# Optimization experiments

Measured on AMD Instinct MI355X. Metric: run time of the kernel, lower is better.

Reference implementation:

```python
import jax, jax.numpy as jnp
import numpy as np
from jax import lax

D_MODEL = 1024
D_STATE = 128
HEADDIM = 64
EXPAND = 2
NGROUPS = 1
CHUNK = 256
D_INNER = EXPAND * D_MODEL          # 2048
D_SSM = D_INNER                      # d_ssm defaults to d_inner
NHEADS = D_SSM // HEADDIM            # 32
CONV_DIM = D_SSM + 2 * NGROUPS * D_STATE   # 2304
D_IN_PROJ = 2 * D_INNER + 2 * NGROUPS * D_STATE + NHEADS  # 4384 -> d_mlp = 0
BATCH = 2
SEQLEN = 2048
EPS = 1e-5


def setup_inputs() -> dict:
    key = jax.random.key(0)
    ks = jax.random.split(key, 9)
    u = jax.random.normal(ks[0], (BATCH, SEQLEN, D_MODEL), jnp.float32)
    # indices into left-padded (len = SEQLEN+1) sequence; 0 selects the zero pad
    conv_indices = jax.random.randint(ks[1], (BATCH, 4 * SEQLEN), 0, SEQLEN + 1)
    W_in = jax.random.normal(ks[2], (D_IN_PROJ, D_MODEL), jnp.float32) / np.sqrt(D_MODEL).astype(np.float32)
    conv_w = jax.random.normal(ks[3], (CONV_DIM, 4), jnp.float32) * 0.2
    conv_b = jax.random.normal(ks[4], (CONV_DIM,), jnp.float32) * 0.02
    # dt_bias init exactly as the module: inverse-softplus of dt in [dt_min, dt_max]
    dt = jnp.exp(jax.random.uniform(ks[5], (NHEADS,), jnp.float32) * (np.log(0.1) - np.log(0.001)) + np.log(0.001))
    dt = jnp.clip(dt, 1e-4)
    dt_bias = dt + jnp.log(-jnp.expm1(-dt))
    A_log = jnp.log(jax.random.uniform(ks[6], (NHEADS,), jnp.float32, minval=1.0, maxval=16.0))
    D = jnp.ones((NHEADS,), jnp.float32)
    norm_w = jnp.ones((D_SSM,), jnp.float32)
    W_out = jax.random.normal(ks[7], (D_MODEL, D_INNER), jnp.float32) / np.sqrt(D_INNER).astype(np.float32)
    return dict(u=u, conv_indices=conv_indices, W_in=W_in, conv_w=conv_w, conv_b=conv_b,
                dt_bias=dt_bias, A_log=A_log, D=D, norm_w=norm_w, W_out=W_out)


def _segsum(x):
    # x: (b, c, h, cs) -> (b, c, h, cs, cs); out[..., t, s] = sum_{k=s+1..t} x[..., k]
    cs = x.shape[-1]
    cx = jnp.cumsum(x, axis=-1)
    diff = cx[..., :, None] - cx[..., None, :]
    mask = jnp.tril(jnp.ones((cs, cs), dtype=bool))
    return jnp.where(mask, diff, -jnp.inf)


def _ssd(x, dt, A, Bh, Ch, D):
    # Mamba2 SSD chunked scan. x:(b,l,h,p), dt:(b,l,h), A:(h,), Bh/Ch:(b,l,h,n), D:(h,)
    b, l, h, p = x.shape
    n = Bh.shape[-1]
    c = l // CHUNK
    xr = x.reshape(b, c, CHUNK, h, p)
    dtr = dt.reshape(b, c, CHUNK, h)
    Br = Bh.reshape(b, c, CHUNK, h, n)
    Cr = Ch.reshape(b, c, CHUNK, h, n)
    dA = dtr * A                                 # (b,c,cs,h)
    Acum = jnp.cumsum(dA, axis=2)                # (b,c,cs,h)
    Lm = jnp.exp(_segsum(jnp.transpose(dA, (0, 1, 3, 2))))  # (b,c,h,cs,cs)
    dtx = xr * dtr[..., None]                    # dt-weighted inputs
    # intra-chunk (diagonal blocks)
    Yd = jnp.einsum('bcthn,bcshn,bchts,bcshp->bcthp', Cr, Br, Lm, dtx)
    # per-chunk final states
    decay_states = jnp.exp(Acum[:, :, -1:, :] - Acum)        # (b,c,cs,h)
    states = jnp.einsum('bcshn,bcsh,bcshp->bchpn', Br, decay_states, dtx)
    chunk_decay = jnp.exp(Acum[:, :, -1, :])     # (b,c,h)
    def step(h_prev, inp):
        dec, st = inp
        return h_prev * dec[..., None, None] + st, h_prev
    init = jnp.zeros((b, h, p, n), x.dtype)
    _, prev = lax.scan(step, init, (jnp.moveaxis(chunk_decay, 1, 0), jnp.moveaxis(states, 1, 0)))
    prev = jnp.moveaxis(prev, 0, 1)              # (b,c,h,p,n): state entering each chunk
    # inter-chunk (off-diagonal) contribution
    Yoff = jnp.einsum('bcthn,bchpn,bcth->bcthp', Cr, prev, jnp.exp(Acum))
    Y = Yd + Yoff + D[None, None, None, :, None] * xr
    return Y.reshape(b, l, h, p)


def reference(u, conv_indices, W_in, conv_w, conv_b, dt_bias, A_log, D, norm_w, W_out):
    b, l, _ = u.shape
    zxbcdt = u @ W_in.T                          # (b,l,4384); d_mlp == 0
    z, xBC, dt_raw = jnp.split(zxbcdt, [D_SSM, D_SSM + CONV_DIM], axis=-1)
    # tree conv: left-pad seq by 1, gather 4 tree positions per output step, depthwise conv k=4 stride=4
    xc = jnp.transpose(xBC, (0, 2, 1))           # (b, conv_dim, l)
    xp = jnp.pad(xc, ((0, 0), (0, 0), (1, 0)))
    idx = jnp.broadcast_to(conv_indices[:, None, :], (b, CONV_DIM, 4 * l))
    g = jnp.take_along_axis(xp, idx, axis=2).reshape(b, CONV_DIM, l, 4)
    conv = jnp.einsum('bclk,ck->bcl', g, conv_w) + conv_b[None, :, None]
    xBC = jax.nn.silu(jnp.transpose(conv, (0, 2, 1)))  # (b,l,conv_dim)
    x, Bm, Cm = jnp.split(xBC, [D_SSM, D_SSM + NGROUPS * D_STATE], axis=-1)
    x = x.reshape(b, l, NHEADS, HEADDIM)
    hpg = NHEADS // NGROUPS
    Bh = jnp.repeat(Bm.reshape(b, l, NGROUPS, D_STATE), hpg, axis=2)
    Ch = jnp.repeat(Cm.reshape(b, l, NGROUPS, D_STATE), hpg, axis=2)
    dt = jax.nn.softplus(dt_raw + dt_bias)       # dt_softplus=True, default dt_limit
    A = -jnp.exp(A_log.astype(jnp.float32))
    y = _ssd(x, dt, A, Bh, Ch, D).reshape(b, l, D_SSM)
    # RMSNormGated, norm_before_gate=False, group_size = d_ssm (ngroups=1)
    yz = y * jax.nn.silu(z)
    var = jnp.mean(jnp.square(yz), axis=-1, keepdims=True)
    y = yz * lax.rsqrt(var + EPS) * norm_w
    return y @ W_out.T
```

## Files before the change

kernel.cpp:

```cpp
#include <hip/hip_runtime.h>

#define BB 2
#define LL 2048
#define DMODEL 1024
#define DSSM 2048
#define NH 32
#define HD 64
#define DST 128
#define CONVD 2304
#define DPROJ 4384
#define CS 64
#define NC 32
#define BLTOT (BB*LL)

typedef short v8s __attribute__((ext_vector_type(8)));
typedef float v4f __attribute__((ext_vector_type(4)));

__device__ __forceinline__ float b2f(unsigned short h) {
  union { unsigned int u; float f; } v; v.u = ((unsigned int)h) << 16; return v.f;
}
__device__ __forceinline__ unsigned short f2b(float f) {
  union { float f; unsigned int u; } v; v.f = f;
  unsigned int u = v.u;
  return (unsigned short)((u + 0x7fffu + ((u >> 16) & 1u)) >> 16);
}
__device__ __forceinline__ v4f mfma16(v8s a, v8s b, v4f c) {
  return __builtin_amdgcn_mfma_f32_16x16x32_bf16(a, b, c, 0, 0, 0);
}
__device__ __forceinline__ void gl_lds16(const unsigned short* g, unsigned short* l) {
  __builtin_amdgcn_global_load_lds(
      (const __attribute__((address_space(1))) void*)(g),
      (__attribute__((address_space(3))) void*)(l), 16, 0, 0);
}

__global__ __launch_bounds__(256) void cvt3_kernel(
    const float* __restrict__ a, unsigned short* __restrict__ oa, int na4,
    const float* __restrict__ b, unsigned short* __restrict__ ob, int nb4,
    const float* __restrict__ c, unsigned short* __restrict__ oc, int nc4)
{
  int i = blockIdx.x * 256 + threadIdx.x;
  const float* src; unsigned short* dst; int j;
  if (i < na4) { src = a; dst = oa; j = i; }
  else if (i < na4 + nb4) { src = b; dst = ob; j = i - na4; }
  else if (i < na4 + nb4 + nc4) { src = c; dst = oc; j = i - na4 - nb4; }
  else return;
  float4 v = ((const float4*)src)[j];
  ushort4 o;
  o.x = f2b(v.x); o.y = f2b(v.y); o.z = f2b(v.z); o.w = f2b(v.w);
  ((ushort4*)dst)[j] = o;
}

template<int TN, int OUT_BF16>
__global__ __launch_bounds__(256) void gemm_bt(
    const unsigned short* __restrict__ A, const unsigned short* __restrict__ Bt,
    void* __restrict__ Cout, int M, int N, int K, int ldc)
{
  constexpr int NT = TN / 32;
  const int bm = blockIdx.x, bn = blockIdx.y;
  const int tid = threadIdx.x;
  const int wave = tid >> 6, lane = tid & 63;
  const int wm = wave & 1, wn = wave >> 1;
  const int q = lane >> 4, lr = lane & 15;

  __shared__ __align__(16) unsigned short As[128 * 64];
  __shared__ __align__(16) unsigned short Bs[TN * 64];

  v4f acc[4][NT];
#pragma unroll
  for (int i = 0; i < 4; i++)
#pragma unroll
    for (int j = 0; j < NT; j++) acc[i][j] = v4f{0.f, 0.f, 0.f, 0.f};

  const int lrow = lane >> 3;
  const int gchunk = (lane & 7) ^ lrow;

  for (int k0 = 0; k0 < K; k0 += 64) {
    __syncthreads();
#pragma unroll
    for (int it = 0; it < 4; ++it) {
      int r = wave * 32 + it * 8 + lrow;
      gl_lds16(A + (size_t)(bm * 128 + r) * K + k0 + gchunk * 8,
               &As[(wave * 32 + it * 8) * 64]);
    }
#pragma unroll
    for (int it = 0; it < TN / 32; ++it) {
      int rloc = wave * (TN / 4) + it * 8;
      int rb = bn * TN + rloc + lrow; if (rb >= N) rb = N - 1;
      gl_lds16(Bt + (size_t)rb * K + k0 + gchunk * 8, &Bs[rloc * 64]);
    }
    __syncthreads();
#pragma unroll
    for (int ks = 0; ks < 64; ks += 32) {
      const int c0 = (ks >> 3) + q;
      v8s af[4], bf[NT];
#pragma unroll
      for (int mt = 0; mt < 4; ++mt) {
        int r = wm * 64 + mt * 16 + lr;
        af[mt] = *(const v8s*)&As[r * 64 + ((c0 ^ (r & 7)) << 3)];
      }
#pragma unroll
      for (int nt = 0; nt < NT; ++nt) {
        int r = wn * (TN / 2) + nt * 16 + lr;
        bf[nt] = *(const v8s*)&Bs[r * 64 + ((c0 ^ (r & 7)) << 3)];
      }
#pragma unroll
      for (int mt = 0; mt < 4; ++mt)
#pragma unroll
        for (int nt = 0; nt < NT; ++nt)
          acc[mt][nt] = mfma16(af[mt], bf[nt], acc[mt][nt]);
    }
  }
#pragma unroll
  for (int mt = 0; mt < 4; ++mt) {
#pragma unroll
    for (int nt = 0; nt < NT; ++nt) {
      int row = bm * 128 + wm * 64 + mt * 16 + q * 4;
      int col = bn * TN + wn * (TN / 2) + nt * 16 + lr;
      if (col < N) {
#pragma unroll
        for (int r = 0; r < 4; ++r) {
          float v = acc[mt][nt][r];
          if (OUT_BF16) ((unsigned short*)Cout)[(size_t)(row + r) * ldc + col] = f2b(v);
          else          ((float*)Cout)[(size_t)(row + r) * ldc + col] = v;
        }
      }
    }
  }
}

__global__ __launch_bounds__(256) void conv_kernel(
    const unsigned short* __restrict__ C1, const int* __restrict__ cidx,
    const float* __restrict__ convw, const float* __restrict__ convb,
    const float* __restrict__ dtbias,
    unsigned short* __restrict__ x16, unsigned short* __restrict__ Bg16,
    unsigned short* __restrict__ Cg16, float* __restrict__ dtb)
{
  int bl0 = blockIdx.x * 4;
  int b = bl0 >> 11;
  int tid = threadIdx.x;
  __shared__ int idxs[16];
  if (tid < 16) {
    int tk = tid >> 2, k = tid & 3;
    idxs[tid] = cidx[b * (4 * LL) + (((bl0 + tk) & 2047) * 4) + k];
  }
  __syncthreads();
  const float4* cw4 = (const float4*)convw;
#pragma unroll
  for (int it = 0; it < 3; ++it) {
    int unit = tid + it * 256;
    if (unit >= CONVD / 4) break;
    int c4 = unit * 4;
    float4 w0 = cw4[c4], w1 = cw4[c4 + 1], w2 = cw4[c4 + 2], w3 = cw4[c4 + 3];
    float4 cb = *(const float4*)(convb + c4);
#pragma unroll
    for (int tk = 0; tk < 4; ++tk) {
      int bl = bl0 + tk;
      ushort4 rv[4];
#pragma unroll
      for (int k = 0; k < 4; ++k) {
        int iv = idxs[tk * 4 + k];
        rv[k] = (iv > 0) ? *(const ushort4*)(C1 + (size_t)(b * LL + iv - 1) * DPROJ + DSSM + c4)
                         : make_ushort4(0, 0, 0, 0);
      }
      float a0 = cb.x + b2f(rv[0].x) * w0.x + b2f(rv[1].x) * w0.y + b2f(rv[2].x) * w0.z + b2f(rv[3].x) * w0.w;
      float a1 = cb.y + b2f(rv[0].y) * w1.x + b2f(rv[1].y) * w1.y + b2f(rv[2].y) * w1.z + b2f(rv[3].y) * w1.w;
      float a2 = cb.z + b2f(rv[0].z) * w2.x + b2f(rv[1].z) * w2.y + b2f(rv[2].z) * w2.z + b2f(rv[3].z) * w2.w;
      float a3 = cb.w + b2f(rv[0].w) * w3.x + b2f(rv[1].w) * w3.y + b2f(rv[2].w) * w3.z + b2f(rv[3].w) * w3.w;
      ushort4 o;
      o.x = f2b(a0 / (1.f + __expf(-a0)));
      o.y = f2b(a1 / (1.f + __expf(-a1)));
      o.z = f2b(a2 / (1.f + __expf(-a2)));
      o.w = f2b(a3 / (1.f + __expf(-a3)));
      if (c4 < DSSM)            *(ushort4*)(x16 + (size_t)bl * DSSM + c4) = o;
      else if (c4 < DSSM + DST) *(ushort4*)(Bg16 + (size_t)bl * DST + (c4 - DSSM)) = o;
      else                      *(ushort4*)(Cg16 + (size_t)bl * DST + (c4 - DSSM - DST)) = o;
    }
  }
  if (tid < 4 * NH) {
    int tk = tid >> 5, hh = tid & 31;
    int bl = bl0 + tk;
    float raw = b2f(C1[(size_t)bl * DPROJ + DSSM + CONVD + hh]) + dtbias[hh];
    float dtv = (raw > 20.f) ? raw : log1pf(__expf(raw));
    dtb[(size_t)bl * NH + hh] = dtv;
  }
}

__global__ __launch_bounds__(256) void d1_intra(
    const unsigned short* __restrict__ x16, const unsigned short* __restrict__ Bg16,
    const unsigned short* __restrict__ Cg16, const float* __restrict__ dtb,
    const float* __restrict__ A_log, const float* __restrict__ Dp,
    unsigned short* __restrict__ y16, unsigned short* __restrict__ statesb,
    float* __restrict__ cdb, float* __restrict__ acumb)
{
  int gid = blockIdx.x;
  int h = gid & 31, ci = (gid >> 5) & 31, b = gid >> 10;
  int tid = threadIdx.x, wave = tid >> 6, lane = tid & 63, q = lane >> 4, lr = lane & 15;

  __shared__ __align__(16) unsigned short BnG[CS * 136];
  __shared__ __align__(16) unsigned short BTw[DST * 72];
  __shared__ __align__(16) unsigned short xT[HD * 72];
  __shared__ float dt_s[CS], ac_s[CS], dec_s[CS];

  const size_t blbase = (size_t)b * LL + ci * CS;
  const size_t chbase = (size_t)(b * NC + ci) * NH + h;
  float Ah = -__expf(A_log[h]);

  if (wave == 0) {
    float d = dtb[(blbase + lane) * NH + h];
    float a = d * Ah;
#pragma unroll
    for (int off = 1; off < 64; off <<= 1) {
      float u = __shfl_up(a, off, 64);
      if (lane >= off) a += u;
    }
    float tot = __shfl(a, 63, 64);
    dt_s[lane] = d;
    ac_s[lane] = a;
    dec_s[lane] = __expf(tot - a);
    acumb[chbase * CS + lane] = a;
    if (lane == 0) cdb[chbase] = __expf(tot);
  }

#pragma unroll
  for (int g = 0; g < 8; ++g) {
    int f = g * 256 + tid;
    int s = f >> 5, c4 = (f & 31) * 4;
    *(ushort4*)&BnG[s * 136 + c4] = *(const ushort4*)(Bg16 + (blbase + s) * DST + c4);
  }
#pragma unroll
  for (int g = 0; g < 4; ++g) {
    int f = g * 256 + tid;
    int s = f >> 4, p4 = (f & 15) * 4;
    ushort4 xv = *(const ushort4*)(x16 + (blbase + s) * DSSM + h * HD + p4);
    xT[(p4 + 0) * 72 + s] = xv.x;
    xT[(p4 + 1) * 72 + s] = xv.y;
    xT[(p4 + 2) * 72 + s] = xv.z;
    xT[(p4 + 3) * 72 + s] = xv.w;
  }
  __syncthreads();

#pragma unroll
  for (int g = 0; g < 4; ++g) {
    int f = g * 256 + tid;
    int n = f >> 3, sg = f & 7;
    int s0 = sg * 8;
    ushort4 lo, hi;
    lo.x = f2b(b2f(BnG[(s0 + 0) * 136 + n]) * dec_s[s0 + 0] * dt_s[s0 + 0]);
    lo.y = f2b(b2f(BnG[(s0 + 1) * 136 + n]) * dec_s[s0 + 1] * dt_s[s0 + 1]);
    lo.z = f2b(b2f(BnG[(s0 + 2) * 136 + n]) * dec_s[s0 + 2] * dt_s[s0 + 2]);
    lo.w = f2b(b2f(BnG[(s0 + 3) * 136 + n]) * dec_s[s0 + 3] * dt_s[s0 + 3]);
    hi.x = f2b(b2f(BnG[(s0 + 4) * 136 + n]) * dec_s[s0 + 4] * dt_s[s0 + 4]);
    hi.y = f2b(b2f(BnG[(s0 + 5) * 136 + n]) * dec_s[s0 + 5] * dt_s[s0 + 5]);
    hi.z = f2b(b2f(BnG[(s0 + 6) * 136 + n]) * dec_s[s0 + 6] * dt_s[s0 + 6]);
    hi.w = f2b(b2f(BnG[(s0 + 7) * 136 + n]) * dec_s[s0 + 7] * dt_s[s0 + 7]);
    *(ushort4*)&BTw[n * 72 + s0] = lo;
    *(ushort4*)&BTw[n * 72 + s0 + 4] = hi;
  }

  v4f accS[4];
#pragma unroll
  for (int i = 0; i < 4; i++) accS[i] = v4f{0.f, 0.f, 0.f, 0.f};
#pragma unroll
  for (int ks = 0; ks < 128; ks += 32) {
    v8s a = *(const v8s*)(Cg16 + (blbase + wave * 16 + lr) * DST + ks + q * 8);
#pragma unroll
    for (int si = 0; si < 4; ++si) {
      v8s bb = *(const v8s*)&BnG[(si * 16 + lr) * 136 + ks + q * 8];
      accS[si] = mfma16(a, bb, accS[si]);
    }
  }
  __syncthreads();

  {
    int tbase = wave * 16 + q * 4;
#pragma unroll
    for (int si = 0; si < 4; ++si) {
      int s = si * 16 + lr;
      float ds = dt_s[s], as = ac_s[s];
#pragma unroll
      for (int r = 0; r < 4; ++r) {
        int tt = tbase + r;
        float g = 0.f;
        if (s <= tt) g = accS[si][r] * __expf(ac_s[tt] - as) * ds;
        BnG[tt * 72 + s] = f2b(g);
      }
    }
  }
  __syncthreads();

  v4f accY[4], accPT[4][2];
#pragma unroll
  for (int i = 0; i < 4; i++) {
    accY[i] = v4f{0.f,0.f,0.f,0.f};
    accPT[i][0] = v4f{0.f,0.f,0.f,0.f};
    accPT[i][1] = v4f{0.f,0.f,0.f,0.f};
  }
  int nw = wave * 32;
#pragma unroll
  for (int ks = 0; ks < 64; ks += 32) {
    v8s xf[4];
#pragma unroll
    for (int i = 0; i < 4; ++i) xf[i] = *(const v8s*)&xT[(i * 16 + lr) * 72 + ks + q * 8];
    v8s aG  = *(const v8s*)&BnG[(wave * 16 + lr) * 72 + ks + q * 8];
    v8s bw0 = *(const v8s*)&BTw[(nw + lr) * 72 + ks + q * 8];
    v8s bw1 = *(const v8s*)&BTw[(nw + 16 + lr) * 72 + ks + q * 8];
#pragma unroll
    for (int nt = 0; nt < 4; ++nt) {
      accY[nt] = mfma16(aG, xf[nt], accY[nt]);
      accPT[nt][0] = mfma16(xf[nt], bw0, accPT[nt][0]);
      accPT[nt][1] = mfma16(xf[nt], bw1, accPT[nt][1]);
    }
  }

  float Dh = Dp[h];
#pragma unroll
  for (int nt = 0; nt < 4; ++nt) {
    int p = nt * 16 + lr;
#pragma unroll
    for (int r = 0; r < 4; ++r) {
      int t = wave * 16 + q * 4 + r;
      float xv = b2f(xT[p * 72 + t]);
      y16[(blbase + t) * DSSM + h * HD + p] = f2b(accY[nt][r] + Dh * xv);
    }
  }
  size_t sbase = chbase * (DST * HD);
#pragma unroll
  for (int mt = 0; mt < 4; ++mt) {
#pragma unroll
    for (int nt = 0; nt < 2; ++nt) {
      int n = nw + nt * 16 + lr;
#pragma unroll
      for (int r = 0; r < 4; ++r) {
        int p = mt * 16 + q * 4 + r;
        statesb[sbase + (size_t)p * DST + n] = f2b(accPT[mt][nt][r]);
      }
    }
  }
}

__global__ __launch_bounds__(256) void d2_scan(
    unsigned short* __restrict__ statesb, const float* __restrict__ cdb)
{
  int g = blockIdx.x;
  int seg = g & 31, bh = g >> 5;
  int b = bh >> 5, h = bh & 31;
  int e = seg * 256 + threadIdx.x;
  const size_t cstride = (size_t)NH * DST * HD;
  size_t base = ((size_t)(b * NC) * NH + h) * (DST * HD) + e;
  unsigned short st[NC];
#pragma unroll
  for (int ci = 0; ci < NC; ++ci) st[ci] = statesb[base + ci * cstride];
  float run = 0.f;
#pragma unroll
  for (int ci = 0; ci < NC; ++ci) {
    float cd = cdb[(b * NC + ci) * NH + h];
    statesb[base + ci * cstride] = f2b(run);
    run = run * cd + b2f(st[ci]);
  }
}

__global__ __launch_bounds__(256) void d3_inter(
    const unsigned short* __restrict__ Cg16,
    const unsigned short* __restrict__ statesb, const float* __restrict__ acumb,
    unsigned short* __restrict__ y16)
{
  int gid = blockIdx.x;
  int h = gid & 31, ci = (gid >> 5) & 31, b = gid >> 10;
  int tid = threadIdx.x, wave = tid >> 6, lane = tid & 63, q = lane >> 4, lr = lane & 15;
  __shared__ __align__(16) unsigned short pT[HD * 136];
  __shared__ __align__(16) float ys[CS * 68];
  __shared__ float ea[CS];
  const size_t blbase = (size_t)b * LL + ci * CS;
  const size_t chbase = (size_t)(b * NC + ci) * NH + h;
  if (tid < CS) ea[tid] = __expf(acumb[chbase * CS + tid]);
  size_t sbase = chbase * (DST * HD);
#pragma unroll
  for (int g = 0; g < 8; ++g) {
    int f = g * 256 + tid;
    int p = f >> 5, c4 = (f & 31) * 4;
    *(ushort4*)&pT[p * 136 + c4] = *(const ushort4*)(statesb + sbase + (size_t)p * DST + c4);
  }
  __syncthreads();
  v4f acc[4];
#pragma unroll
  for (int i = 0; i < 4; i++) acc[i] = v4f{0.f, 0.f, 0.f, 0.f};
#pragma unroll
  for (int ks = 0; ks < 128; ks += 32) {
    v8s a = *(const v8s*)(Cg16 + (blbase + wave * 16 + lr) * DST + ks + q * 8);
#pragma unroll
    for (int nt = 0; nt < 4; ++nt) {
      v8s bb = *(const v8s*)&pT[(nt * 16 + lr) * 136 + ks + q * 8];
      acc[nt] = mfma16(a, bb, acc[nt]);
    }
  }
#pragma unroll
  for (int nt = 0; nt < 4; ++nt) {
#pragma unroll
    for (int r = 0; r < 4; ++r)
      ys[(wave * 16 + q * 4 + r) * 68 + nt * 16 + lr] = acc[nt][r];
  }
  __syncthreads();
#pragma unroll
  for (int it = 0; it < 2; ++it) {
    int unit = it * 256 + tid;
    int t = unit >> 3, p8 = (unit & 7) * 8;
    float ea_t = ea[t];
    size_t off = (blbase + t) * DSSM + h * HD + p8;
    uint4 yv = *(const uint4*)(y16 + off);
    float4 o0 = *(const float4*)&ys[t * 68 + p8];
    float4 o1 = *(const float4*)&ys[t * 68 + p8 + 4];
    const unsigned int* yu = (const unsigned int*)&yv;
    float oo[8] = {o0.x, o0.y, o0.z, o0.w, o1.x, o1.y, o1.z, o1.w};
    unsigned int ro[4];
#pragma unroll
    for (int d = 0; d < 4; ++d) {
      unsigned short y0 = (unsigned short)(yu[d] & 0xffffu), y1 = (unsigned short)(yu[d] >> 16);
      float v0 = b2f(y0) + ea_t * oo[d * 2 + 0];
      float v1 = b2f(y1) + ea_t * oo[d * 2 + 1];
      ro[d] = (unsigned int)f2b(v0) | ((unsigned int)f2b(v1) << 16);
    }
    *(uint4*)(y16 + off) = make_uint4(ro[0], ro[1], ro[2], ro[3]);
  }
}

__global__ __launch_bounds__(256) void norm_kernel(
    const unsigned short* __restrict__ y16, const unsigned short* __restrict__ C1,
    const float* __restrict__ normw, unsigned short* __restrict__ yzn)
{
  int bl = blockIdx.x;
  int tid = threadIdx.x;
  int wave = tid >> 6, lane = tid & 63;
  int c8 = tid * 8;
  uint4 yv = *(const uint4*)(y16 + (size_t)bl * DSSM + c8);
  uint4 zv = *(const uint4*)(C1 + (size_t)bl * DPROJ + c8);
  const unsigned int* yu = (const unsigned int*)&yv;
  const unsigned int* zu = (const unsigned int*)&zv;
  float vals[8];
  float ss = 0.f;
#pragma unroll
  for (int d = 0; d < 4; ++d) {
    unsigned short y0 = (unsigned short)(yu[d] & 0xffffu), y1 = (unsigned short)(yu[d] >> 16);
    unsigned short z0 = (unsigned short)(zu[d] & 0xffffu), z1 = (unsigned short)(zu[d] >> 16);
    float zf0 = b2f(z0), zf1 = b2f(z1);
    float v0 = b2f(y0) * (zf0 / (1.f + __expf(-zf0)));
    float v1 = b2f(y1) * (zf1 / (1.f + __expf(-zf1)));
    vals[d * 2] = v0; vals[d * 2 + 1] = v1;
    ss += v0 * v0 + v1 * v1;
  }
#pragma unroll
  for (int off = 32; off > 0; off >>= 1) ss += __shfl_down(ss, off);
  __shared__ float red[4];
  if (lane == 0) red[wave] = ss;
  __syncthreads();
  float tot = red[0] + red[1] + red[2] + red[3];
  float scale = rsqrtf(tot * (1.f / 2048.f) + 1e-5f);
  float4 w0 = *(const float4*)(normw + c8);
  float4 w1 = *(const float4*)(normw + c8 + 4);
  float ws[8] = {w0.x, w0.y, w0.z, w0.w, w1.x, w1.y, w1.z, w1.w};
  unsigned int ro[4];
#pragma unroll
  for (int d = 0; d < 4; ++d) {
    unsigned short r0 = f2b(vals[d * 2] * scale * ws[d * 2]);
    unsigned short r1 = f2b(vals[d * 2 + 1] * scale * ws[d * 2 + 1]);
    ro[d] = (unsigned int)r0 | ((unsigned int)r1 << 16);
  }
  *(uint4*)(yzn + (size_t)bl * DSSM + c8) = make_uint4(ro[0], ro[1], ro[2], ro[3]);
}

extern "C" void kernel_launch(void* const* d_in, const int* in_sizes, int n_in,
                              void* d_out, int out_size, void* d_ws, size_t ws_size,
                              hipStream_t stream) {
  const float* u      = (const float*)d_in[0];
  const int*   cidx   = (const int*)d_in[1];
  const float* W_in   = (const float*)d_in[2];
  const float* convw  = (const float*)d_in[3];
  const float* convb  = (const float*)d_in[4];
  const float* dtbias = (const float*)d_in[5];
  const float* A_log  = (const float*)d_in[6];
  const float* Dp     = (const float*)d_in[7];
  const float* normw  = (const float*)d_in[8];
  const float* W_out  = (const float*)d_in[9];

  char* w = (char*)d_ws;
  size_t off = 0;
  auto alloc = [&](size_t bytes) { char* p = w + off; off += (bytes + 255) & ~(size_t)255; return p; };
  unsigned short* u16     = (unsigned short*)alloc((size_t)BLTOT * DMODEL * 2);
  unsigned short* Win16   = (unsigned short*)alloc((size_t)DPROJ * DMODEL * 2);
  unsigned short* Wout16  = (unsigned short*)alloc((size_t)DMODEL * DSSM * 2);
  unsigned short* C1      = (unsigned short*)alloc((size_t)BLTOT * DPROJ * 2);
  unsigned short* x16     = (unsigned short*)alloc((size_t)BLTOT * DSSM * 2);
  unsigned short* Bg16    = (unsigned short*)alloc((size_t)BLTOT * DST * 2);
  unsigned short* Cg16    = (unsigned short*)alloc((size_t)BLTOT * DST * 2);
  float*          dtb     = (float*)alloc((size_t)BLTOT * NH * 4);
  float*          acumb   = (float*)alloc((size_t)BB * NC * NH * CS * 4);
  unsigned short* y16     = (unsigned short*)alloc((size_t)BLTOT * DSSM * 2);
  unsigned short* statesb = (unsigned short*)alloc((size_t)BB * NC * NH * DST * HD * 2);
  float*          cdb     = (float*)alloc((size_t)BB * NC * NH * 4);
  unsigned short* yzn     = (unsigned short*)alloc((size_t)BLTOT * DSSM * 2);

  const int na4 = BLTOT * DMODEL / 4, nb4 = DPROJ * DMODEL / 4, nc4 = DMODEL * DSSM / 4;
  cvt3_kernel<<<(na4 + nb4 + nc4 + 255) / 256, 256, 0, stream>>>(
      u, u16, na4, W_in, Win16, nb4, W_out, Wout16, nc4);

  gemm_bt<128, 1><<<dim3(BLTOT / 128, (DPROJ + 127) / 128), 256, 0, stream>>>(
      u16, Win16, C1, BLTOT, DPROJ, DMODEL, DPROJ);
  conv_kernel<<<BLTOT / 4, 256, 0, stream>>>(C1, cidx, convw, convb, dtbias, x16, Bg16, Cg16, dtb);
  d1_intra<<<BB * NC * NH, 256, 0, stream>>>(x16, Bg16, Cg16, dtb, A_log, Dp, y16, statesb, cdb, acumb);
  d2_scan<<<BB * NH * 32, 256, 0, stream>>>(statesb, cdb);
  d3_inter<<<BB * NC * NH, 256, 0, stream>>>(Cg16, statesb, acumb, y16);
  norm_kernel<<<BLTOT, 256, 0, stream>>>(y16, C1, normw, yzn);
  gemm_bt<64, 0><<<dim3(BLTOT / 128, DMODEL / 64), 256, 0, stream>>>(
      yzn, Wout16, (float*)d_out, BLTOT, DMODEL, DSSM, DMODEL);
}
```

Before: 263.0 us.

## Add 8-wave triple-buffered 256x128 GEMM for input projection

Adds a new GEMM kernel with 512 threads, 256x128 output tiles and a three-stage LDS buffer that uses direct global-to-LDS loads. Loads for tile k+2 are interleaved between the two MFMA halves of tile k, with s_setprio raised around the MFMAs, so memory latency is hidden behind compute. The input-projection GEMM now uses this kernel in place of the older 128x128 one. The cost is more LDS (about 144KB per block) and fewer blocks, which lowers occupancy and can leave CUs idle on the tail wave.

Measured after the change: 271.7 us. 3.3% more time.

```diff
diff --git a/kernel.cpp b/kernel.cpp
--- a/kernel.cpp
+++ b/kernel.cpp
@@ -116,6 +116,121 @@
     for (int nt = 0; nt < NT; ++nt) {
       int row = bm * 128 + wm * 64 + mt * 16 + q * 4;
       int col = bn * TN + wn * (TN / 2) + nt * 16 + lr;
+      if (col < N) {
+#pragma unroll
+        for (int r = 0; r < 4; ++r) {
+          float v = acc[mt][nt][r];
+          if (OUT_BF16) ((unsigned short*)Cout)[(size_t)(row + r) * ldc + col] = f2b(v);
+          else          ((float*)Cout)[(size_t)(row + r) * ldc + col] = v;
+        }
+      }
+    }
+  }
+}
+
+#define STAGE_A8(buf, kt2, j) \
+  gl_lds16(A + (size_t)(bm * 256 + (j) * 64 + wave * 8 + lrow) * K + (size_t)(kt2) * 64 + gchunk * 8, \
+           &As[buf][((j) * 64 + wave * 8) * 64])
+#define STAGE_B8(buf, kt2, j) do { \
+  int rb_ = bn * 128 + (j) * 64 + wave * 8 + lrow; if (rb_ >= N) rb_ = N - 1; \
+  gl_lds16(Bt + (size_t)rb_ * K + (size_t)(kt2) * 64 + gchunk * 8, \
+           &Bs[buf][((j) * 64 + wave * 8) * 64]); } while (0)
+
+template<int OUT_BF16>
+__global__ __launch_bounds__(512, 2) void gemm8p(
+    const unsigned short* __restrict__ A, const unsigned short* __restrict__ Bt,
+    void* __restrict__ Cout, int M, int N, int K, int ldc)
+{
+  const int bm = blockIdx.x, bn = blockIdx.y;
+  const int tid = threadIdx.x;
+  const int wave = tid >> 6, lane = tid & 63;
+  const int wm = wave >> 1, wn = wave & 1;
+  const int q = lane >> 4, lr = lane & 15;
+  const int lrow = lane >> 3;
+  const int gchunk = (lane & 7) ^ lrow;
+
+  __shared__ __align__(16) unsigned short As[3][256 * 64];
+  __shared__ __align__(16) unsigned short Bs[3][128 * 64];
+
+  const int nkt = K >> 6;
+
+  v4f acc[4][4];
+#pragma unroll
+  for (int i = 0; i < 4; i++)
+#pragma unroll
+    for (int j = 0; j < 4; j++) acc[i][j] = v4f{0.f, 0.f, 0.f, 0.f};
+
+#pragma unroll
+  for (int j = 0; j < 4; ++j) STAGE_A8(0, 0, j);
+  STAGE_B8(0, 0, 0); STAGE_B8(0, 0, 1);
+#pragma unroll
+  for (int j = 0; j < 4; ++j) STAGE_A8(1, 1, j);
+  STAGE_B8(1, 1, 0); STAGE_B8(1, 1, 1);
+  asm volatile("s_waitcnt vmcnt(6)" ::: "memory");
+  __builtin_amdgcn_s_barrier();
+
+  int cb = 0;
+  for (int kt = 0; kt < nkt; ++kt) {
+    const int sb = (cb + 2 >= 3) ? cb - 1 : cb + 2;
+    const bool do_stage = (kt + 2) < nkt;
+    const unsigned short* __restrict__ Ab = As[cb];
+    const unsigned short* __restrict__ Bb = Bs[cb];
+    v8s af[4], bf[4];
+
+#pragma unroll
+    for (int mt = 0; mt < 4; ++mt) {
+      int r = wm * 64 + mt * 16 + lr;
+      af[mt] = *(const v8s*)&Ab[r * 64 + ((q ^ (r & 7)) << 3)];
+    }
+#pragma unroll
+    for (int nt = 0; nt < 4; ++nt) {
+      int r = wn * 64 + nt * 16 + lr;
+      bf[nt] = *(const v8s*)&Bb[r * 64 + ((q ^ (r & 7)) << 3)];
+    }
+    if (do_stage) { STAGE_A8(sb, kt + 2, 0); STAGE_A8(sb, kt + 2, 1); STAGE_A8(sb, kt + 2, 2); }
+    __builtin_amdgcn_s_barrier();
+    __builtin_amdgcn_s_setprio(1);
+#pragma unroll
+    for (int mt = 0; mt < 4; ++mt)
+#pragma unroll
+      for (int nt = 0; nt < 4; ++nt)
+        acc[mt][nt] = mfma16(af[mt], bf[nt], acc[mt][nt]);
+    __builtin_amdgcn_s_setprio(0);
+    __builtin_amdgcn_s_barrier();
+
+#pragma unroll
+    for (int mt = 0; mt < 4; ++mt) {
+      int r = wm * 64 + mt * 16 + lr;
+      af[mt] = *(const v8s*)&Ab[r * 64 + (((4 + q) ^ (r & 7)) << 3)];
+    }
+#pragma unroll
+    for (int nt = 0; nt < 4; ++nt) {
+      int r = wn * 64 + nt * 16 + lr;
+      bf[nt] = *(const v8s*)&Bb[r * 64 + (((4 + q) ^ (r & 7)) << 3)];
+    }
+    if (do_stage) { STAGE_A8(sb, kt + 2, 3); STAGE_B8(sb, kt + 2, 0); STAGE_B8(sb, kt + 2, 1); }
+    __builtin_amdgcn_s_barrier();
+    __builtin_amdgcn_s_setprio(1);
+#pragma unroll
+    for (int mt = 0; mt < 4; ++mt)
+#pragma unroll
+      for (int nt = 0; nt < 4; ++nt)
+        acc[mt][nt] = mfma16(af[mt], bf[nt], acc[mt][nt]);
+    __builtin_amdgcn_s_setprio(0);
+    if (kt + 1 < nkt) {
+      if (do_stage) { asm volatile("s_waitcnt vmcnt(6)" ::: "memory"); }
+      else          { asm volatile("s_waitcnt vmcnt(0)" ::: "memory"); }
+    }
+    __builtin_amdgcn_s_barrier();
+    cb = (cb + 1 >= 3) ? 0 : cb + 1;
+  }
+
+#pragma unroll
+  for (int mt = 0; mt < 4; ++mt) {
+#pragma unroll
+    for (int nt = 0; nt < 4; ++nt) {
+      int row = bm * 256 + wm * 64 + mt * 16 + q * 4;
+      int col = bn * 128 + wn * 64 + nt * 16 + lr;
       if (col < N) {
 #pragma unroll
         for (int r = 0; r < 4; ++r) {
@@ -502,7 +617,7 @@
   cvt3_kernel<<<(na4 + nb4 + nc4 + 255) / 256, 256, 0, stream>>>(
       u, u16, na4, W_in, Win16, nb4, W_out, Wout16, nc4);
 
-  gemm_bt<128, 1><<<dim3(BLTOT / 128, (DPROJ + 127) / 128), 256, 0, stream>>>(
+  gemm8p<1><<<dim3(BLTOT / 256, (DPROJ + 127) / 128), 512, 0, stream>>>(
       u16, Win16, C1, BLTOT, DPROJ, DMODEL, DPROJ);
   conv_kernel<<<BLTOT / 4, 256, 0, stream>>>(C1, cidx, convw, convb, dtbias, x16, Bg16, Cg16, dtb);
   d1_intra<<<BB * NC * NH, 256, 0, stream>>>(x16, Bg16, Cg16, dtb, A_log, Dp, y16, statesb, cdb, acumb);
```

## Fuse x-channel conv into SSD intra kernel, swizzle GEMM blocks, stage bf16 epilogue

Applied to the files above, without the earlier changes.

The depthwise gather-conv and SiLU for the x channels move from the standalone conv kernel into d1_intra, which now builds its transposed x tile straight from C1. This removes the x16 intermediate write and read. The conv kernel now handles only the B/C and dt channels, with 16 timesteps per block. Both GEMMs get a block-index swizzle for L2 locality, and the bf16-output GEMM stages its tile through XOR-swizzled shared memory to issue 16-byte coalesced stores. The trade-off is that d1_intra gathers C1 rows indirectly per head and uses more shared memory, and the swizzle hardcodes 32 M-blocks.

New measurement: 265.1 us. About the same (+0.8%).

```diff
diff --git a/kernel.cpp b/kernel.cpp
--- a/kernel.cpp
+++ b/kernel.cpp
@@ -56,14 +56,18 @@
     void* __restrict__ Cout, int M, int N, int K, int ldc)
 {
   constexpr int NT = TN / 32;
-  const int bm = blockIdx.x, bn = blockIdx.y;
+  const int lin = blockIdx.y * 32 + blockIdx.x;
+  const int cpx = (gridDim.x * gridDim.y) >> 3;
+  const int swz = (lin & 7) * cpx + (lin >> 3);
+  const int bm = swz & 31, bn = swz >> 5;
   const int tid = threadIdx.x;
   const int wave = tid >> 6, lane = tid & 63;
   const int wm = wave & 1, wn = wave >> 1;
   const int q = lane >> 4, lr = lane & 15;
 
-  __shared__ __align__(16) unsigned short As[128 * 64];
-  __shared__ __align__(16) unsigned short Bs[TN * 64];
+  __shared__ __align__(16) unsigned short smem[128 * 64 + TN * 64];
+  unsigned short* As = smem;
+  unsigned short* Bs = smem + 128 * 64;
 
   v4f acc[4][NT];
 #pragma unroll
@@ -110,74 +114,99 @@
           acc[mt][nt] = mfma16(af[mt], bf[nt], acc[mt][nt]);
     }
   }
-#pragma unroll
-  for (int mt = 0; mt < 4; ++mt) {
-#pragma unroll
-    for (int nt = 0; nt < NT; ++nt) {
-      int row = bm * 128 + wm * 64 + mt * 16 + q * 4;
-      int col = bn * TN + wn * (TN / 2) + nt * 16 + lr;
-      if (col < N) {
+
+  if constexpr (OUT_BF16) {
+    __syncthreads();
+    unsigned short* Cs = smem;
+#pragma unroll
+    for (int mt = 0; mt < 4; ++mt) {
+#pragma unroll
+      for (int nt = 0; nt < NT; ++nt) {
+        int col = wn * (TN / 2) + nt * 16 + lr;
 #pragma unroll
         for (int r = 0; r < 4; ++r) {
-          float v = acc[mt][nt][r];
-          if (OUT_BF16) ((unsigned short*)Cout)[(size_t)(row + r) * ldc + col] = f2b(v);
-          else          ((float*)Cout)[(size_t)(row + r) * ldc + col] = v;
+          int row = wm * 64 + mt * 16 + q * 4 + r;
+          int baddr = (row * (TN * 2) + col * 2) ^ ((row & 7) << 4);
+          *(unsigned short*)((char*)Cs + baddr) = f2b(acc[mt][nt][r]);
         }
       }
     }
-  }
-}
-
-__global__ __launch_bounds__(256) void conv_kernel(
+    __syncthreads();
+    constexpr int CHR = TN / 8;
+#pragma unroll
+    for (int u = tid; u < 128 * CHR; u += 256) {
+      int row = u / CHR, ch = u % CHR;
+      int baddr = row * (TN * 2) + ((ch ^ (row & 7)) << 4);
+      uint4 v = *(const uint4*)((const char*)Cs + baddr);
+      int gcol = bn * TN + ch * 8;
+      if (gcol < N)
+        *(uint4*)((unsigned short*)Cout + (size_t)(bm * 128 + row) * ldc + gcol) = v;
+    }
+  } else {
+#pragma unroll
+    for (int mt = 0; mt < 4; ++mt) {
+#pragma unroll
+      for (int nt = 0; nt < NT; ++nt) {
+        int row = bm * 128 + wm * 64 + mt * 16 + q * 4;
+        int col = bn * TN + wn * (TN / 2) + nt * 16 + lr;
+        if (col < N) {
+#pragma unroll
+          for (int r = 0; r < 4; ++r)
+            ((float*)Cout)[(size_t)(row + r) * ldc + col] = acc[mt][nt][r];
+        }
+      }
+    }
+  }
+}
+
+__global__ __launch_bounds__(256) void convBC_kernel(
     const unsigned short* __restrict__ C1, const int* __restrict__ cidx,
     const float* __restrict__ convw, const float* __restrict__ convb,
     const float* __restrict__ dtbias,
-    unsigned short* __restrict__ x16, unsigned short* __restrict__ Bg16,
-    unsigned short* __restrict__ Cg16, float* __restrict__ dtb)
-{
-  int bl0 = blockIdx.x * 4;
+    unsigned short* __restrict__ Bg16, unsigned short* __restrict__ Cg16,
+    float* __restrict__ dtb)
+{
+  int bl0 = blockIdx.x * 16;
   int b = bl0 >> 11;
   int tid = threadIdx.x;
-  __shared__ int idxs[16];
-  if (tid < 16) {
+  __shared__ int idxs[64];
+  if (tid < 64) {
     int tk = tid >> 2, k = tid & 3;
     idxs[tid] = cidx[b * (4 * LL) + (((bl0 + tk) & 2047) * 4) + k];
   }
   __syncthreads();
   const float4* cw4 = (const float4*)convw;
-#pragma unroll
-  for (int it = 0; it < 3; ++it) {
-    int unit = tid + it * 256;
-    if (unit >= CONVD / 4) break;
-    int c4 = unit * 4;
-    float4 w0 = cw4[c4], w1 = cw4[c4 + 1], w2 = cw4[c4 + 2], w3 = cw4[c4 + 3];
-    float4 cb = *(const float4*)(convb + c4);
-#pragma unroll
-    for (int tk = 0; tk < 4; ++tk) {
-      int bl = bl0 + tk;
-      ushort4 rv[4];
-#pragma unroll
-      for (int k = 0; k < 4; ++k) {
-        int iv = idxs[tk * 4 + k];
-        rv[k] = (iv > 0) ? *(const ushort4*)(C1 + (size_t)(b * LL + iv - 1) * DPROJ + DSSM + c4)
-                         : make_ushort4(0, 0, 0, 0);
-      }
-      float a0 = cb.x + b2f(rv[0].x) * w0.x + b2f(rv[1].x) * w0.y + b2f(rv[2].x) * w0.z + b2f(rv[3].x) * w0.w;
-      float a1 = cb.y + b2f(rv[0].y) * w1.x + b2f(rv[1].y) * w1.y + b2f(rv[2].y) * w1.z + b2f(rv[3].y) * w1.w;
-      float a2 = cb.z + b2f(rv[0].z) * w2.x + b2f(rv[1].z) * w2.y + b2f(rv[2].z) * w2.z + b2f(rv[3].z) * w2.w;
-      float a3 = cb.w + b2f(rv[0].w) * w3.x + b2f(rv[1].w) * w3.y + b2f(rv[2].w) * w3.z + b2f(rv[3].w) * w3.w;
-      ushort4 o;
-      o.x = f2b(a0 / (1.f + __expf(-a0)));
-      o.y = f2b(a1 / (1.f + __expf(-a1)));
-      o.z = f2b(a2 / (1.f + __expf(-a2)));
-      o.w = f2b(a3 / (1.f + __expf(-a3)));
-      if (c4 < DSSM)            *(ushort4*)(x16 + (size_t)bl * DSSM + c4) = o;
-      else if (c4 < DSSM + DST) *(ushort4*)(Bg16 + (size_t)bl * DST + (c4 - DSSM)) = o;
-      else                      *(ushort4*)(Cg16 + (size_t)bl * DST + (c4 - DSSM - DST)) = o;
-    }
-  }
-  if (tid < 4 * NH) {
-    int tk = tid >> 5, hh = tid & 31;
+  int quad = tid & 63;
+  int relc = DSSM + quad * 4;
+  float4 w0 = cw4[relc], w1 = cw4[relc + 1], w2 = cw4[relc + 2], w3 = cw4[relc + 3];
+  float4 cb = *(const float4*)(convb + relc);
+  int tk0 = (tid >> 6) * 4;
+#pragma unroll
+  for (int tt = 0; tt < 4; ++tt) {
+    int tk = tk0 + tt;
+    int bl = bl0 + tk;
+    ushort4 rv[4];
+#pragma unroll
+    for (int k = 0; k < 4; ++k) {
+      int iv = idxs[tk * 4 + k];
+      rv[k] = (iv > 0) ? *(const ushort4*)(C1 + (size_t)(b * LL + iv - 1) * DPROJ + DSSM + relc)
+                       : make_ushort4(0, 0, 0, 0);
+    }
+    float a0 = cb.x + b2f(rv[0].x) * w0.x + b2f(rv[1].x) * w0.y + b2f(rv[2].x) * w0.z + b2f(rv[3].x) * w0.w;
+    float a1 = cb.y + b2f(rv[0].y) * w1.x + b2f(rv[1].y) * w1.y + b2f(rv[2].y) * w1.z + b2f(rv[3].y) * w1.w;
+    float a2 = cb.z + b2f(rv[0].z) * w2.x + b2f(rv[1].z) * w2.y + b2f(rv[2].z) * w2.z + b2f(rv[3].z) * w2.w;
+    float a3 = cb.w + b2f(rv[0].w) * w3.x + b2f(rv[1].w) * w3.y + b2f(rv[2].w) * w3.z + b2f(rv[3].w) * w3.w;
+    ushort4 o;
+    o.x = f2b(a0 / (1.f + __expf(-a0)));
+    o.y = f2b(a1 / (1.f + __expf(-a1)));
+    o.z = f2b(a2 / (1.f + __expf(-a2)));
+    o.w = f2b(a3 / (1.f + __expf(-a3)));
+    int cc = relc - DSSM;
+    if (cc < DST) *(ushort4*)(Bg16 + (size_t)bl * DST + cc) = o;
+    else          *(ushort4*)(Cg16 + (size_t)bl * DST + (cc - DST)) = o;
+  }
+  for (int u = tid; u < 16 * NH; u += 256) {
+    int tk = u >> 5, hh = u & 31;
     int bl = bl0 + tk;
     float raw = b2f(C1[(size_t)bl * DPROJ + DSSM + CONVD + hh]) + dtbias[hh];
     float dtv = (raw > 20.f) ? raw : log1pf(__expf(raw));
@@ -186,7 +215,9 @@
 }
 
 __global__ __launch_bounds__(256) void d1_intra(
-    const unsigned short* __restrict__ x16, const unsigned short* __restrict__ Bg16,
+    const unsigned short* __restrict__ C1, const int* __restrict__ cidx,
+    const float* __restrict__ convw, const float* __restrict__ convb,
+    const unsigned short* __restrict__ Bg16,
     const unsigned short* __restrict__ Cg16, const float* __restrict__ dtb,
     const float* __restrict__ A_log, const float* __restrict__ Dp,
     unsigned short* __restrict__ y16, unsigned short* __restrict__ statesb,
@@ -200,6 +231,9 @@
   __shared__ __align__(16) unsigned short BTw[DST * 72];
   __shared__ __align__(16) unsigned short xT[HD * 72];
   __shared__ float dt_s[CS], ac_s[CS], dec_s[CS];
+  __shared__ int idxs[CS * 4];
+  __shared__ float wls[HD * 4];
+  __shared__ float bls[HD];
 
   const size_t blbase = (size_t)b * LL + ci * CS;
   const size_t chbase = (size_t)(b * NC + ci) * NH + h;
@@ -227,16 +261,12 @@
     int s = f >> 5, c4 = (f & 31) * 4;
     *(ushort4*)&BnG[s * 136 + c4] = *(const ushort4*)(Bg16 + (blbase + s) * DST + c4);
   }
-#pragma unroll
-  for (int g = 0; g < 4; ++g) {
-    int f = g * 256 + tid;
-    int s = f >> 4, p4 = (f & 15) * 4;
-    ushort4 xv = *(const ushort4*)(x16 + (blbase + s) * DSSM + h * HD + p4);
-    xT[(p4 + 0) * 72 + s] = xv.x;
-    xT[(p4 + 1) * 72 + s] = xv.y;
-    xT[(p4 + 2) * 72 + s] = xv.z;
-    xT[(p4 + 3) * 72 + s] = xv.w;
-  }
+  {
+    int s = tid >> 2, k = tid & 3;
+    idxs[tid] = cidx[b * (4 * LL) + (ci * CS + s) * 4 + k];
+  }
+  if (tid < HD) *(float4*)&wls[tid * 4] = *(const float4*)(convw + (h * HD + tid) * 4);
+  if (tid < HD / 4) *(float4*)&bls[tid * 4] = *(const float4*)(convb + h * HD + tid * 4);
   __syncthreads();
 
 #pragma unroll
@@ -269,6 +299,31 @@
       accS[si] = mfma16(a, bb, accS[si]);
     }
   }
+
+#pragma unroll
+  for (int g = 0; g < 4; ++g) {
+    int f = g * 256 + tid;
+    int s = f >> 4, p4 = (f & 15) * 4;
+    ushort4 rv[4];
+#pragma unroll
+    for (int k = 0; k < 4; ++k) {
+      int iv = idxs[s * 4 + k];
+      rv[k] = (iv > 0) ? *(const ushort4*)(C1 + (size_t)(b * LL + iv - 1) * DPROJ + DSSM + h * HD + p4)
+                       : make_ushort4(0, 0, 0, 0);
+    }
+    float4 w0 = *(const float4*)&wls[(p4 + 0) * 4];
+    float4 w1 = *(const float4*)&wls[(p4 + 1) * 4];
+    float4 w2 = *(const float4*)&wls[(p4 + 2) * 4];
+    float4 w3 = *(const float4*)&wls[(p4 + 3) * 4];
+    float a0 = bls[p4 + 0] + b2f(rv[0].x) * w0.x + b2f(rv[1].x) * w0.y + b2f(rv[2].x) * w0.z + b2f(rv[3].x) * w0.w;
+    float a1 = bls[p4 + 1] + b2f(rv[0].y) * w1.x + b2f(rv[1].y) * w1.y + b2f(rv[2].y) * w1.z + b2f(rv[3].y) * w1.w;
+    float a2 = bls[p4 + 2] + b2f(rv[0].z) * w2.x + b2f(rv[1].z) * w2.y + b2f(rv[2].z) * w2.z + b2f(rv[3].z) * w2.w;
+    float a3 = bls[p4 + 3] + b2f(rv[0].w) * w3.x + b2f(rv[1].w) * w3.y + b2f(rv[2].w) * w3.z + b2f(rv[3].w) * w3.w;
+    xT[(p4 + 0) * 72 + s] = f2b(a0 / (1.f + __expf(-a0)));
+    xT[(p4 + 1) * 72 + s] = f2b(a1 / (1.f + __expf(-a1)));
+    xT[(p4 + 2) * 72 + s] = f2b(a2 / (1.f + __expf(-a2)));
+    xT[(p4 + 3) * 72 + s] = f2b(a3 / (1.f + __expf(-a3)));
+  }
   __syncthreads();
 
   {
@@ -488,7 +543,6 @@
   unsigned short* Win16   = (unsigned short*)alloc((size_t)DPROJ * DMODEL * 2);
   unsigned short* Wout16  = (unsigned short*)alloc((size_t)DMODEL * DSSM * 2);
   unsigned short* C1      = (unsigned short*)alloc((size_t)BLTOT * DPROJ * 2);
-  unsigned short* x16     = (unsigned short*)alloc((size_t)BLTOT * DSSM * 2);
   unsigned short* Bg16    = (unsigned short*)alloc((size_t)BLTOT * DST * 2);
   unsigned short* Cg16    = (unsigned short*)alloc((size_t)BLTOT * DST * 2);
   float*          dtb     = (float*)alloc((size_t)BLTOT * NH * 4);
@@ -504,8 +558,9 @@
 
   gemm_bt<128, 1><<<dim3(BLTOT / 128, (DPROJ + 127) / 128), 256, 0, stream>>>(
       u16, Win16, C1, BLTOT, DPROJ, DMODEL, DPROJ);
-  conv_kernel<<<BLTOT / 4, 256, 0, stream>>>(C1, cidx, convw, convb, dtbias, x16, Bg16, Cg16, dtb);
-  d1_intra<<<BB * NC * NH, 256, 0, stream>>>(x16, Bg16, Cg16, dtb, A_log, Dp, y16, statesb, cdb, acumb);
+  convBC_kernel<<<BLTOT / 16, 256, 0, stream>>>(C1, cidx, convw, convb, dtbias, Bg16, Cg16, dtb);
+  d1_intra<<<BB * NC * NH, 256, 0, stream>>>(C1, cidx, convw, convb, Bg16, Cg16, dtb,
+                                             A_log, Dp, y16, statesb, cdb, acumb);
   d2_scan<<<BB * NH * 32, 256, 0, stream>>>(statesb, cdb);
   d3_inter<<<BB * NC * NH, 256, 0, stream>>>(Cg16, statesb, acumb, y16);
   norm_kernel<<<BLTOT, 256, 0, stream>>>(y16, C1, normw, yzn);
```
